# Optimization experiments

Hardware: AMD Instinct MI355X
Metric: run time of the kernel (lower is better)

The kernel has to match this reference:

```python
import jax, jax.numpy as jnp
import numpy as np

V = 32000      # vocab_size
CTX = 1024     # context_length
D = 768        # n_embd
H = 12         # n_heads
HD = D // H    # head_dim
L = 6          # n_layers
DFF = 4 * D
B, S = 2, 1024
EPS = 1e-5


def _layernorm(x, w, b):
    mu = jnp.mean(x, axis=-1, keepdims=True)
    var = jnp.mean(jnp.square(x - mu), axis=-1, keepdims=True)
    return (x - mu) * jax.lax.rsqrt(var + EPS) * w + b


def setup_inputs() -> dict:
    key = jax.random.key(0)
    ks = iter(jax.random.split(key, 32))
    s = 0.02
    idx = jax.random.randint(next(ks), (B, S), 0, V)
    p = {
        "idx": idx,
        "tok_emb": jax.random.normal(next(ks), (V, D), jnp.float32) * s,
        "pos_emb": jax.random.normal(next(ks), (CTX, D), jnp.float32) * s,
        "ln1_w": jnp.ones((L, D)), "ln1_b": jnp.zeros((L, D)),
        "Wq": jax.random.normal(next(ks), (L, D, D), jnp.float32) * s,
        "bq": jnp.zeros((L, D)),
        "Wk": jax.random.normal(next(ks), (L, D, D), jnp.float32) * s,
        "bk": jnp.zeros((L, D)),
        "Wv": jax.random.normal(next(ks), (L, D, D), jnp.float32) * s,
        "bv": jnp.zeros((L, D)),
        "Wo": jax.random.normal(next(ks), (L, D, D), jnp.float32) * s,
        "bo": jnp.zeros((L, D)),
        "ln2_w": jnp.ones((L, D)), "ln2_b": jnp.zeros((L, D)),
        "W1": jax.random.normal(next(ks), (L, D, DFF), jnp.float32) * s,
        "b1": jnp.zeros((L, DFF)),
        "W2": jax.random.normal(next(ks), (L, DFF, D), jnp.float32) * s,
        "b2": jnp.zeros((L, D)),
        "lnf_w": jnp.ones((D,)), "lnf_b": jnp.zeros((D,)),
        "lm_head_w": jax.random.normal(next(ks), (D, V), jnp.float32) * s,
    }
    return p


def _forward(idx, tok_emb, pos_emb, ln1_w, ln1_b, Wq, bq, Wk, bk, Wv, bv,
             Wo, bo, ln2_w, ln2_b, W1, b1, W2, b2, lnf_w, lnf_b, lm_head_w):
    b, s = idx.shape
    x = tok_emb[idx] + pos_emb[:s]  # [B,S,D]
    mask = jnp.tril(jnp.ones((s, s), dtype=bool))  # causal
    scale = 1.0 / np.sqrt(HD)
    for l in range(L):
        # --- attention ---
        h = _layernorm(x, ln1_w[l], ln1_b[l])
        q = (h @ Wq[l] + bq[l]).reshape(b, s, H, HD).transpose(0, 2, 1, 3)
        k = (h @ Wk[l] + bk[l]).reshape(b, s, H, HD).transpose(0, 2, 1, 3)
        v = (h @ Wv[l] + bv[l]).reshape(b, s, H, HD).transpose(0, 2, 1, 3)
        att = jnp.einsum('bhqd,bhkd->bhqk', q, k) * scale
        att = jnp.where(mask, att, -jnp.inf)
        att = jax.nn.softmax(att, axis=-1)
        y = jnp.einsum('bhqk,bhkd->bhqd', att, v)
        y = y.transpose(0, 2, 1, 3).reshape(b, s, D)
        x = x + y @ Wo[l] + bo[l]
        # --- MLP ---
        h2 = _layernorm(x, ln2_w[l], ln2_b[l])
        x = x + jax.nn.relu(h2 @ W1[l] + b1[l]) @ W2[l] + b2[l]
    logits = _layernorm(x, lnf_w, lnf_b) @ lm_head_w  # [B,S,V]
    return logits


def reference(idx, tok_emb, pos_emb, ln1_w, ln1_b, Wq, bq, Wk, bk, Wv, bv,
              Wo, bo, ln2_w, ln2_b, W1, b1, W2, b2, lnf_w, lnf_b, lm_head_w):
    return _forward(idx, tok_emb, pos_emb, ln1_w, ln1_b, Wq, bq, Wk, bk, Wv,
                    bv, Wo, bo, ln2_w, ln2_b, W1, b1, W2, b2, lnf_w, lnf_b,
                    lm_head_w)
```

## Files before the change

### kernel.cpp

```cpp
#include <hip/hip_runtime.h>
#include <hip/hip_bf16.h>
#include <math.h>

#define D 768
#define NH 12
#define HD 64
#define NL 6
#define DFF 3072
#define BB 2
#define SS 1024
#define NROWS (BB*SS)
#define VOCAB 32000
#define QKVN (3*D)
#define LN_EPS 1e-5f

typedef __attribute__((ext_vector_type(8))) short bf16x8;
typedef __attribute__((ext_vector_type(4))) float f32x4;

typedef __attribute__((address_space(1))) const unsigned char* gas_ptr;
typedef __attribute__((address_space(3))) unsigned char* las_ptr;

__device__ __forceinline__ void load_lds16(const void* g, void* l) {
    __builtin_amdgcn_global_load_lds((gas_ptr)g, (las_ptr)l, 16, 0, 0);
}

__device__ __forceinline__ void storeOut(float* p, float v) { *p = v; }
__device__ __forceinline__ void storeOut(__hip_bfloat16* p, float v) { *p = __float2bfloat16(v); }
__device__ __forceinline__ ushort f2bs(float f) {
    __hip_bfloat16 h = __float2bfloat16(f);
    return *(ushort*)&h;
}

#define WAIT_VMCNT(n) asm volatile("s_waitcnt vmcnt(" #n ")" ::: "memory")

__global__ void embed_kernel(const int* __restrict__ idx, const float* __restrict__ tok,
                             const float* __restrict__ pos, float* __restrict__ x) {
    int row = blockIdx.x;
    int s = row % SS;
    int t = idx[row];
    for (int c = threadIdx.x; c < D; c += blockDim.x)
        x[row*D + c] = tok[(size_t)t*D + c] + pos[s*D + c];
}

template<typename OT>
__global__ __launch_bounds__(256) void layernorm_kernel(const float* __restrict__ x,
                                                        const float* __restrict__ w,
                                                        const float* __restrict__ b,
                                                        OT* __restrict__ out) {
    int row = blockIdx.x;
    __shared__ float l1[4], l2[4];
    int base = row * D;
    float vals[3];
    float s1 = 0.f, s2 = 0.f;
#pragma unroll
    for (int i = 0; i < 3; i++) {
        float v = x[base + threadIdx.x + i*256];
        vals[i] = v; s1 += v; s2 += v*v;
    }
#pragma unroll
    for (int o = 32; o > 0; o >>= 1) {
        s1 += __shfl_down(s1, o, 64);
        s2 += __shfl_down(s2, o, 64);
    }
    if ((threadIdx.x & 63) == 0) { l1[threadIdx.x >> 6] = s1; l2[threadIdx.x >> 6] = s2; }
    __syncthreads();
    float sum   = l1[0] + l1[1] + l1[2] + l1[3];
    float sumsq = l2[0] + l2[1] + l2[2] + l2[3];
    float mu  = sum * (1.f / D);
    float var = sumsq * (1.f / D) - mu * mu;
    float inv = rsqrtf(var + LN_EPS);
#pragma unroll
    for (int i = 0; i < 3; i++) {
        int c = threadIdx.x + i*256;
        storeOut(&out[base + c], (vals[i] - mu) * inv * w[c] + b[c]);
    }
}

__global__ __launch_bounds__(256) void transpose_cvt(const float* __restrict__ src,
                                                     __hip_bfloat16* __restrict__ dst,
                                                     int K, int N,
                                                     size_t srcLayerStride, size_t dstLayerStride,
                                                     int dstRowOff) {
    int l = blockIdx.z;
    src += (size_t)l * srcLayerStride;
    dst += (size_t)l * dstLayerStride + (size_t)dstRowOff * K;
    __shared__ float t[32][33];
    int k0 = blockIdx.x*32, n0 = blockIdx.y*32;
    int tx = threadIdx.x & 31, ty = threadIdx.x >> 5;
    for (int i = ty; i < 32; i += 8) t[i][tx] = src[(size_t)(k0+i)*N + n0+tx];
    __syncthreads();
    for (int i = ty; i < 32; i += 8) dst[(size_t)(n0+i)*K + k0+tx] = __float2bfloat16(t[tx][i]);
}

__global__ __launch_bounds__(256) void qkvo_trans(const float* __restrict__ Wq,
                                                  const float* __restrict__ Wk,
                                                  const float* __restrict__ Wv,
                                                  const float* __restrict__ Wo,
                                                  __hip_bfloat16* __restrict__ qkvT,
                                                  __hip_bfloat16* __restrict__ WoT) {
    int z = blockIdx.z, l = z >> 2, m = z & 3;
    const float* src = (m==0 ? Wq : m==1 ? Wk : m==2 ? Wv : Wo) + (size_t)l*D*D;
    __hip_bfloat16* dst = (m < 3) ? qkvT + (size_t)l*QKVN*D + (size_t)m*D*D
                                  : WoT  + (size_t)l*D*D;
    __shared__ float t[32][33];
    int k0 = blockIdx.x*32, n0 = blockIdx.y*32;
    int tx = threadIdx.x & 31, ty = threadIdx.x >> 5;
    for (int i = ty; i < 32; i += 8) t[i][tx] = src[(size_t)(k0+i)*D + n0+tx];
    __syncthreads();
    for (int i = ty; i < 32; i += 8) dst[(size_t)(n0+i)*D + k0+tx] = __float2bfloat16(t[tx][i]);
}

__global__ void pack_qkv_bias(const float* __restrict__ bq, const float* __restrict__ bk,
                              const float* __restrict__ bv, float* __restrict__ dst) {
    int l = blockIdx.y;
    int i = blockIdx.x*256 + threadIdx.x;
    dst[l*QKVN + i]         = bq[l*D + i];
    dst[l*QKVN + D + i]     = bk[l*D + i];
    dst[l*QKVN + 2*D + i]   = bv[l*D + i];
}

#define GSTAGE(buf, k0) do {                                                     \
    _Pragma("unroll")                                                            \
    for (int i_ = 0; i_ < BM/64; i_++) {                                         \
        int rt_ = wid*(BM/4) + i_*16;                                            \
        load_lds16(A + (size_t)(bm + rt_ + lrow)*K + (k0) + lcol,                \
                   &As[buf][rt_][0]);                                            \
    }                                                                            \
    _Pragma("unroll")                                                            \
    for (int i_ = 0; i_ < BN/64; i_++) {                                         \
        int rt_ = wid*(BN/4) + i_*16;                                            \
        load_lds16(BT + (size_t)(bn + rt_ + lrow)*K + (k0) + lcol,               \
                   &Bs[buf][rt_][0]);                                            \
    } } while (0)

template<int BM, int BN, int CMAJ, typename OT, int RELU, int RESID, int HASB, int VSTORE>
__global__ __launch_bounds__(256) void gemm_mfma(const ushort* __restrict__ A,
                                                 const ushort* __restrict__ BT,
                                                 const float* __restrict__ bias,
                                                 const float* __restrict__ X,
                                                 OT* __restrict__ C,
                                                 ushort* __restrict__ vt,
                                                 int N, int K, int gx, int gy) {
    constexpr int WTM = BM/2, WTN = BN/2;
    constexpr int FRM = BM/32, FRN = BN/32;
    __shared__ ushort As[2][BM][32];
    __shared__ ushort Bs[2][BN][32];

    int id = blockIdx.x;
    int swz = (id & 7) * (gridDim.x >> 3) + (id >> 3);
    int bx, by;
    if (CMAJ) { bx = swz / gy; by = swz - bx * gy; }
    else      { by = swz / gx; bx = swz - by * gx; }
    int bm = by * BM, bn = bx * BN;

    int tid = threadIdx.x;
    int lane = tid & 63, wid = tid >> 6;
    int wr = wid >> 1, wc = wid & 1;
    int lrow = lane >> 2;
    int lcol = (((lane & 3) ^ (lrow & 3)) * 8);
    int fr = lane & 15, fc = lane >> 4;

    f32x4 acc[FRM][FRN];
#pragma unroll
    for (int i = 0; i < FRM; i++)
#pragma unroll
        for (int j = 0; j < FRN; j++)
#pragma unroll
            for (int r = 0; r < 4; r++) acc[i][j][r] = 0.f;

    GSTAGE(0, 0);
    asm volatile("s_waitcnt vmcnt(0)" ::: "memory");
    __syncthreads();

    int cur = 0;
    for (int t = 0; t < K/32; t++) {
        if (t*32 + 32 < K) GSTAGE(cur^1, t*32 + 32);
        bf16x8 af[FRM], bf[FRN];
#pragma unroll
        for (int mi = 0; mi < FRM; mi++)
            af[mi] = *(const bf16x8*)&As[cur][wr*WTM + mi*16 + fr][(fc ^ (fr & 3))*8];
#pragma unroll
        for (int ni = 0; ni < FRN; ni++)
            bf[ni] = *(const bf16x8*)&Bs[cur][wc*WTN + ni*16 + fr][(fc ^ (fr & 3))*8];
        __builtin_amdgcn_s_setprio(1);
#pragma unroll
        for (int mi = 0; mi < FRM; mi++)
#pragma unroll
            for (int ni = 0; ni < FRN; ni++)
                acc[mi][ni] = __builtin_amdgcn_mfma_f32_16x16x32_bf16(af[mi], bf[ni], acc[mi][ni], 0, 0, 0);
        __builtin_amdgcn_s_setprio(0);
        asm volatile("s_waitcnt vmcnt(0)" ::: "memory");
        __syncthreads();
        cur ^= 1;
    }

    if (VSTORE && bn >= 2*D) {
        int hh = (bn - 2*D) / HD;
        int b  = bm >> 10;
        size_t vbase = ((size_t)(b*NH + hh)) * HD;
        int srow0 = (bm & (SS-1)) + wr*WTM + fc*4;
#pragma unroll
        for (int mi = 0; mi < FRM; mi++) {
#pragma unroll
            for (int ni = 0; ni < FRN; ni++) {
                int col = bn + wc*WTN + ni*16 + fr;
                int d   = wc*WTN + ni*16 + fr;
                float bv_ = bias[col];
                ushort4 u;
                u.x = f2bs(acc[mi][ni][0] + bv_);
                u.y = f2bs(acc[mi][ni][1] + bv_);
                u.z = f2bs(acc[mi][ni][2] + bv_);
                u.w = f2bs(acc[mi][ni][3] + bv_);
                *(ushort4*)&vt[(vbase + d)*SS + srow0 + mi*16] = u;
            }
        }
    } else {
#pragma unroll
        for (int mi = 0; mi < FRM; mi++) {
#pragma unroll
            for (int r = 0; r < 4; r++) {
                int row = bm + wr*WTM + mi*16 + fc*4 + r;
#pragma unroll
                for (int ni = 0; ni < FRN; ni++) {
                    int col = bn + wc*WTN + ni*16 + fr;
                    float v = acc[mi][ni][r];
                    if (HASB) v += bias[col];
                    if (RESID) v += X[(size_t)row * N + col];
                    if (RELU) v = fmaxf(v, 0.f);
                    storeOut(&C[(size_t)row * N + col], v);
                }
            }
        }
    }
}

#define LGS(buf, k0) do {                                                         \
    _Pragma("unroll")                                                             \
    for (int i_ = 0; i_ < 4; i_++) {                                              \
        int li_ = i_*512 + tid;                                                   \
        int row_ = li_ >> 3;                                                      \
        int kc_ = ((li_ & 7) ^ (row_ & 7)) * 8;                                   \
        size_t doff_ = (size_t)(i_*512 + wid*64) * 8;                             \
        load_lds16(A  + (size_t)(bm + row_)*D + (k0) + kc_,                       \
                   (ushort*)As + (size_t)(buf)*256*64 + doff_);                   \
        load_lds16(BT + (size_t)(bn + row_)*D + (k0) + kc_,                       \
                   (ushort*)Bs + (size_t)(buf)*256*64 + doff_);                   \
    } } while (0)

__global__ __launch_bounds__(512) void lm256_gemm(const ushort* __restrict__ A,
                                                  const ushort* __restrict__ BT,
                                                  float* __restrict__ C) {
    constexpr int NT = D / 64;
    __shared__ ushort As[2][256][64];
    __shared__ ushort Bs[2][256][64];

    int id = blockIdx.x;
    int swz = (id & 7) * 125 + (id >> 3);
    int by = swz & 7;
    int bx = swz >> 3;
    int bm = by * 256, bn = bx * 256;

    int tid = threadIdx.x;
    int lane = tid & 63, wid = tid >> 6;
    int wr = wid >> 2, wc = wid & 3;
    int fr = lane & 15, fc = lane >> 4;

    f32x4 acc[8][4];
#pragma unroll
    for (int i = 0; i < 8; i++)
#pragma unroll
        for (int j = 0; j < 4; j++)
#pragma unroll
            for (int r = 0; r < 4; r++) acc[i][j][r] = 0.f;

    LGS(0, 0);
    LGS(1, 64);
    WAIT_VMCNT(8);
    __builtin_amdgcn_s_barrier();

    for (int t = 0; t < NT; t++) {
        int buf = t & 1;
        bf16x8 bfr[2][4];
#pragma unroll
        for (int kk = 0; kk < 2; kk++)
#pragma unroll
            for (int ni = 0; ni < 4; ni++)
                bfr[kk][ni] = *(const bf16x8*)&Bs[buf][wc*64 + ni*16 + fr][((kk*4 + fc) ^ (fr & 7))*8];
        __builtin_amdgcn_s_setprio(1);
#pragma unroll
        for (int mi = 0; mi < 8; mi++) {
            bf16x8 a0 = *(const bf16x8*)&As[buf][wr*128 + mi*16 + fr][((0 + fc) ^ (fr & 7))*8];
            bf16x8 a1 = *(const bf16x8*)&As[buf][wr*128 + mi*16 + fr][((4 + fc) ^ (fr & 7))*8];
#pragma unroll
            for (int ni = 0; ni < 4; ni++) {
                acc[mi][ni] = __builtin_amdgcn_mfma_f32_16x16x32_bf16(a0, bfr[0][ni], acc[mi][ni], 0, 0, 0);
                acc[mi][ni] = __builtin_amdgcn_mfma_f32_16x16x32_bf16(a1, bfr[1][ni], acc[mi][ni], 0, 0, 0);
            }
        }
        __builtin_amdgcn_s_setprio(0);
        __builtin_amdgcn_s_barrier();
        asm volatile("" ::: "memory");
        if (t + 2 < NT) LGS(buf, (t+2)*64);
        if (t + 1 < NT) {
            if (t + 2 < NT) WAIT_VMCNT(8);
            else            WAIT_VMCNT(0);
            __builtin_amdgcn_s_barrier();
        }
    }

#pragma unroll
    for (int mi = 0; mi < 8; mi++)
#pragma unroll
        for (int r = 0; r < 4; r++) {
            int row = bm + wr*128 + mi*16 + fc*4 + r;
            float* cp = C + (size_t)row * VOCAB + bn + wc*64 + fr;
#pragma unroll
            for (int ni = 0; ni < 4; ni++)
                cp[ni*16] = acc[mi][ni][r];
        }
}

#define KVSTAGE(buf, kv0) do {                                                   \
    _Pragma("unroll")                                                            \
    for (int j_ = 0; j_ < 2; j_++) {                                             \
        int r_ = w*16 + j_*8 + srow8;                                            \
        load_lds16(qkv + (size_t)(b*SS + (kv0) + r_)*QKVN + D + h*HD + schunk*8, \
                   &Ks[buf][w*16 + j_*8][0]);                                    \
        load_lds16(vt + ((size_t)(b*NH + h)*HD + r_)*SS + (kv0) + schunk*8,      \
                   &Vs[buf][w*16 + j_*8][0]);                                    \
    } } while (0)

__global__ __launch_bounds__(256) void attn_mfma(const ushort* __restrict__ qkv,
                                                 const ushort* __restrict__ vt,
                                                 __hip_bfloat16* __restrict__ y) {
    const int bx = blockIdx.x;
    const int qt = 15 - (bx & 15);
    const int h  = (bx >> 4) % NH;
    const int b  = bx / (16*NH);
    const int tid  = threadIdx.x;
    const int lane = tid & 63, w = tid >> 6;
    const int fr = lane & 15, fc = lane >> 4;

    __shared__ ushort Qs[64][64];
    __shared__ ushort Ks[2][64][64];
    __shared__ ushort Vs[2][64][64];
    __shared__ ushort Ps[4][16][72];

    const int q0 = qt * 64;
    const int srow8  = lane >> 3;
    const int schunk = (lane & 7) ^ srow8;

#pragma unroll
    for (int j = 0; j < 2; j++) {
        int r = w*16 + j*8 + srow8;
        load_lds16(qkv + (size_t)(b*SS + q0 + r)*QKVN + h*HD + schunk*8, &Qs[w*16 + j*8][0]);
    }
    KVSTAGE(0, 0);
    asm volatile("s_waitcnt vmcnt(0)" ::: "memory");
    __syncthreads();
    bf16x8 qf[2];
#pragma unroll
    for (int s = 0; s < 2; s++)
        qf[s] = *(const bf16x8*)&Qs[w*16 + fr][((s*4 + fc) ^ (fr & 7))*8];

    f32x4 oacc[4];
#pragma unroll
    for (int ni = 0; ni < 4; ni++)
#pragma unroll
        for (int r = 0; r < 4; r++) oacc[ni][r] = 0.f;
    float m[4] = {-INFINITY, -INFINITY, -INFINITY, -INFINITY};
    float l[4] = {0.f, 0.f, 0.f, 0.f};

    int cur = 0;
    for (int kt = 0; kt <= qt; kt++) {
        if (kt < qt) KVSTAGE(cur^1, (kt+1)*64);
        f32x4 sacc[4];
#pragma unroll
        for (int ni = 0; ni < 4; ni++)
#pragma unroll
            for (int r = 0; r < 4; r++) sacc[ni][r] = 0.f;
#pragma unroll
        for (int ni = 0; ni < 4; ni++)
#pragma unroll
            for (int s = 0; s < 2; s++) {
                bf16x8 kf = *(const bf16x8*)&Ks[cur][ni*16 + fr][((s*4 + fc) ^ (fr & 7))*8];
                sacc[ni] = __builtin_amdgcn_mfma_f32_16x16x32_bf16(qf[s], kf, sacc[ni], 0, 0, 0);
            }
        if (kt == qt) {
#pragma unroll
            for (int ni = 0; ni < 4; ni++)
#pragma unroll
                for (int r = 0; r < 4; r++) {
                    float v = sacc[ni][r] * 0.125f;
                    sacc[ni][r] = (ni*16 + fr > w*16 + fc*4 + r) ? -INFINITY : v;
                }
        } else {
#pragma unroll
            for (int ni = 0; ni < 4; ni++)
#pragma unroll
                for (int r = 0; r < 4; r++) sacc[ni][r] *= 0.125f;
        }
        float p[4][4];
#pragma unroll
        for (int r = 0; r < 4; r++) {
            float mx = fmaxf(fmaxf(sacc[0][r], sacc[1][r]), fmaxf(sacc[2][r], sacc[3][r]));
#pragma unroll
            for (int o = 1; o < 16; o <<= 1) mx = fmaxf(mx, __shfl_xor(mx, o, 64));
            float mn = fmaxf(m[r], mx);
            float fac = __expf(m[r] - mn);
            float rs = 0.f;
#pragma unroll
            for (int ni = 0; ni < 4; ni++) {
                float pv = __expf(sacc[ni][r] - mn);
                p[ni][r] = pv;
                rs += pv;
            }
#pragma unroll
            for (int o = 1; o < 16; o <<= 1) rs += __shfl_xor(rs, o, 64);
            l[r] = l[r] * fac + rs;
            m[r] = mn;
#pragma unroll
            for (int ni = 0; ni < 4; ni++) oacc[ni][r] *= fac;
        }
#pragma unroll
        for (int ni = 0; ni < 4; ni++)
#pragma unroll
            for (int r = 0; r < 4; r++)
                Ps[w][fc*4 + r][ni*16 + fr] = f2bs(p[ni][r]);
        bf16x8 pa[2];
#pragma unroll
        for (int s = 0; s < 2; s++) pa[s] = *(const bf16x8*)&Ps[w][fr][s*32 + fc*8];
#pragma unroll
        for (int ni = 0; ni < 4; ni++)
#pragma unroll
            for (int s = 0; s < 2; s++) {
                bf16x8 vf = *(const bf16x8*)&Vs[cur][ni*16 + fr][((s*4 + fc) ^ (fr & 7))*8];
                oacc[ni] = __builtin_amdgcn_mfma_f32_16x16x32_bf16(pa[s], vf, oacc[ni], 0, 0, 0);
            }
        asm volatile("s_waitcnt vmcnt(0)" ::: "memory");
        __syncthreads();
        cur ^= 1;
    }
#pragma unroll
    for (int r = 0; r < 4; r++) {
        float rinv = 1.f / l[r];
        int row = b*SS + q0 + w*16 + fc*4 + r;
#pragma unroll
        for (int ni = 0; ni < 4; ni++)
            y[(size_t)row*D + h*HD + ni*16 + fr] = __float2bfloat16(oacc[ni][r] * rinv);
    }
}

extern "C" void kernel_launch(void* const* d_in, const int* in_sizes, int n_in,
                              void* d_out, int out_size, void* d_ws, size_t ws_size,
                              hipStream_t stream) {
    const int*   idx  = (const int*)d_in[0];
    const float* tok  = (const float*)d_in[1];
    const float* pos  = (const float*)d_in[2];
    const float* ln1w = (const float*)d_in[3];
    const float* ln1b = (const float*)d_in[4];
    const float* Wq   = (const float*)d_in[5];
    const float* bq   = (const float*)d_in[6];
    const float* Wk   = (const float*)d_in[7];
    const float* bk   = (const float*)d_in[8];
    const float* Wv   = (const float*)d_in[9];
    const float* bv   = (const float*)d_in[10];
    const float* Wo   = (const float*)d_in[11];
    const float* bo   = (const float*)d_in[12];
    const float* ln2w = (const float*)d_in[13];
    const float* ln2b = (const float*)d_in[14];
    const float* W1   = (const float*)d_in[15];
    const float* b1   = (const float*)d_in[16];
    const float* W2   = (const float*)d_in[17];
    const float* b2   = (const float*)d_in[18];
    const float* lnfw = (const float*)d_in[19];
    const float* lnfb = (const float*)d_in[20];
    const float* lmw  = (const float*)d_in[21];
    float* out = (float*)d_out;

    char* p = (char*)d_ws;
    __hip_bfloat16* qkvT = (__hip_bfloat16*)p; p += (size_t)NL*QKVN*D*2;
    __hip_bfloat16* WoT  = (__hip_bfloat16*)p; p += (size_t)NL*D*D*2;
    __hip_bfloat16* W1T  = (__hip_bfloat16*)p; p += (size_t)NL*DFF*D*2;
    __hip_bfloat16* W2T  = (__hip_bfloat16*)p; p += (size_t)NL*D*DFF*2;
    __hip_bfloat16* lmT  = (__hip_bfloat16*)p; p += (size_t)VOCAB*D*2;
    float*          bqkv = (float*)p;          p += (size_t)NL*QKVN*4;
    float*          x    = (float*)p;          p += (size_t)NROWS*D*4;
    __hip_bfloat16* h    = (__hip_bfloat16*)p; p += (size_t)NROWS*D*2;
    __hip_bfloat16* qkv  = (__hip_bfloat16*)p; p += (size_t)NROWS*QKVN*2;
    __hip_bfloat16* vt   = (__hip_bfloat16*)p; p += (size_t)BB*NH*HD*SS*2;
    __hip_bfloat16* yb   = (__hip_bfloat16*)p; p += (size_t)NROWS*D*2;
    __hip_bfloat16* a1   = (__hip_bfloat16*)p; p += (size_t)NROWS*DFF*2;

    qkvo_trans<<<dim3(D/32, D/32, NL*4), 256, 0, stream>>>(Wq, Wk, Wv, Wo, qkvT, WoT);
    transpose_cvt<<<dim3(D/32, DFF/32, NL), 256, 0, stream>>>(W1, W1T, D, DFF, (size_t)D*DFF, (size_t)DFF*D, 0);
    transpose_cvt<<<dim3(DFF/32, D/32, NL), 256, 0, stream>>>(W2, W2T, DFF, D, (size_t)DFF*D, (size_t)D*DFF, 0);
    transpose_cvt<<<dim3(D/32, VOCAB/32, 1), 256, 0, stream>>>(lmw, lmT, D, VOCAB, 0, 0, 0);
    pack_qkv_bias<<<dim3(3, NL), 256, 0, stream>>>(bq, bk, bv, bqkv);

    embed_kernel<<<NROWS, 256, 0, stream>>>(idx, tok, pos, x);

    for (int l = 0; l < NL; l++) {
        layernorm_kernel<<<NROWS, 256, 0, stream>>>(x, ln1w + l*D, ln1b + l*D, h);
        gemm_mfma<128,64,0,__hip_bfloat16,0,0,1,1><<<576, 256, 0, stream>>>(
            (const ushort*)h, (const ushort*)(qkvT + (size_t)l*QKVN*D),
            bqkv + (size_t)l*QKVN, nullptr, qkv, (ushort*)vt, QKVN, D, QKVN/64, NROWS/128);
        attn_mfma<<<BB*NH*(SS/64), 256, 0, stream>>>((const ushort*)qkv, (const ushort*)vt, yb);
        gemm_mfma<64,64,0,float,0,1,1,0><<<384, 256, 0, stream>>>(
            (const ushort*)yb, (const ushort*)(WoT + (size_t)l*D*D),
            bo + (size_t)l*D, x, x, nullptr, D, D, D/64, NROWS/64);
        layernorm_kernel<<<NROWS, 256, 0, stream>>>(x, ln2w + l*D, ln2b + l*D, h);
        gemm_mfma<128,128,0,__hip_bfloat16,1,0,1,0><<<384, 256, 0, stream>>>(
            (const ushort*)h, (const ushort*)(W1T + (size_t)l*DFF*D),
            b1 + (size_t)l*DFF, nullptr, a1, nullptr, DFF, D, DFF/128, NROWS/128);
        gemm_mfma<64,64,0,float,0,1,1,0><<<384, 256, 0, stream>>>(
            (const ushort*)a1, (const ushort*)(W2T + (size_t)l*D*DFF),
            b2 + (size_t)l*D, x, x, nullptr, D, DFF, D/64, NROWS/64);
    }
    layernorm_kernel<<<NROWS, 256, 0, stream>>>(x, lnfw, lnfb, h);
    lm256_gemm<<<1000, 512, 0, stream>>>((const ushort*)h, (const ushort*)lmT, out);
}
```

Measured before the change: 1.243 ms.

## Use 4-slot LDS ring pipelines for residual and LM-head GEMMs with new swizzle

```diff
diff --git a/kernel.cpp b/kernel.cpp
--- a/kernel.cpp
+++ b/kernel.cpp
@@ -119,6 +119,7 @@
     dst[l*QKVN + 2*D + i]   = bv[l*D + i];
 }
 
+
 #define GSTAGE(buf, k0) do {                                                     \
     _Pragma("unroll")                                                            \
     for (int i_ = 0; i_ < BM/64; i_++) {                                         \
@@ -157,8 +158,9 @@
     int lane = tid & 63, wid = tid >> 6;
     int wr = wid >> 1, wc = wid & 1;
     int lrow = lane >> 2;
-    int lcol = (((lane & 3) ^ (lrow & 3)) * 8);
+    int lcol = (((lane & 3) ^ ((lane >> 3) & 3)) * 8);
     int fr = lane & 15, fc = lane >> 4;
+    int rchunk = (fc ^ ((fr >> 1) & 3)) * 8;
 
     f32x4 acc[FRM][FRN];
 #pragma unroll
@@ -178,10 +180,10 @@
         bf16x8 af[FRM], bf[FRN];
 #pragma unroll
         for (int mi = 0; mi < FRM; mi++)
-            af[mi] = *(const bf16x8*)&As[cur][wr*WTM + mi*16 + fr][(fc ^ (fr & 3))*8];
+            af[mi] = *(const bf16x8*)&As[cur][wr*WTM + mi*16 + fr][rchunk];
 #pragma unroll
         for (int ni = 0; ni < FRN; ni++)
-            bf[ni] = *(const bf16x8*)&Bs[cur][wc*WTN + ni*16 + fr][(fc ^ (fr & 3))*8];
+            bf[ni] = *(const bf16x8*)&Bs[cur][wc*WTN + ni*16 + fr][rchunk];
         __builtin_amdgcn_s_setprio(1);
 #pragma unroll
         for (int mi = 0; mi < FRM; mi++)
@@ -234,25 +236,106 @@
     }
 }
 
-#define LGS(buf, k0) do {                                                         \
+#define RSTAGE(slot, k0) do {                                                    \
+    int row_ = tid >> 2;                                                         \
+    load_lds16(A  + (size_t)(bm + row_)*K + (k0) + sc_,                          \
+               (char*)As + (size_t)(slot)*4096 + (size_t)wid*1024);              \
+    load_lds16(BT + (size_t)(bn + row_)*K + (k0) + sc_,                          \
+               (char*)Bs + (size_t)(slot)*4096 + (size_t)wid*1024);              \
+    } while (0)
+
+template<int RELU>
+__global__ __launch_bounds__(256) void gemm_ring64(const ushort* __restrict__ A,
+                                                   const ushort* __restrict__ BT,
+                                                   const float* __restrict__ bias,
+                                                   const float* __restrict__ X,
+                                                   float* __restrict__ C,
+                                                   int N, int K, int gx) {
+    __shared__ ushort As[4][64][32];
+    __shared__ ushort Bs[4][64][32];
+
+    int id = blockIdx.x;
+    int swz = (id & 7) * (gridDim.x >> 3) + (id >> 3);
+    int by = swz / gx, bx = swz - by * gx;
+    int bm = by * 64, bn = bx * 64;
+
+    int tid = threadIdx.x;
+    int lane = tid & 63, wid = tid >> 6;
+    int wr = wid >> 1, wc = wid & 1;
+    int sc_ = ((lane & 3) ^ ((lane >> 3) & 3)) * 8;
+    int fr = lane & 15, fc = lane >> 4;
+    int rchunk = (fc ^ ((fr >> 1) & 3)) * 8;
+
+    f32x4 acc[2][2];
+#pragma unroll
+    for (int i = 0; i < 2; i++)
+#pragma unroll
+        for (int j = 0; j < 2; j++)
+#pragma unroll
+            for (int r = 0; r < 4; r++) acc[i][j][r] = 0.f;
+
+    const int NT = K / 32;
+    RSTAGE(0, 0);
+    RSTAGE(1, 32);
+    RSTAGE(2, 64);
+
+    for (int t = 0; t < NT; t++) {
+        if (t < NT-2)      WAIT_VMCNT(4);
+        else if (t == NT-2) WAIT_VMCNT(2);
+        else               WAIT_VMCNT(0);
+        __builtin_amdgcn_s_barrier();
+        asm volatile("" ::: "memory");
+        if (t + 3 < NT) RSTAGE((t+3) & 3, (t+3)*32);
+        int s = t & 3;
+        bf16x8 af[2], bf[2];
+#pragma unroll
+        for (int mi = 0; mi < 2; mi++)
+            af[mi] = *(const bf16x8*)&As[s][wr*32 + mi*16 + fr][rchunk];
+#pragma unroll
+        for (int ni = 0; ni < 2; ni++)
+            bf[ni] = *(const bf16x8*)&Bs[s][wc*32 + ni*16 + fr][rchunk];
+        __builtin_amdgcn_s_setprio(1);
+#pragma unroll
+        for (int mi = 0; mi < 2; mi++)
+#pragma unroll
+            for (int ni = 0; ni < 2; ni++)
+                acc[mi][ni] = __builtin_amdgcn_mfma_f32_16x16x32_bf16(af[mi], bf[ni], acc[mi][ni], 0, 0, 0);
+        __builtin_amdgcn_s_setprio(0);
+    }
+
+#pragma unroll
+    for (int mi = 0; mi < 2; mi++) {
+#pragma unroll
+        for (int r = 0; r < 4; r++) {
+            int row = bm + wr*32 + mi*16 + fc*4 + r;
+#pragma unroll
+            for (int ni = 0; ni < 2; ni++) {
+                int col = bn + wc*32 + ni*16 + fr;
+                float v = acc[mi][ni][r] + bias[col] + X[(size_t)row * N + col];
+                if (RELU) v = fmaxf(v, 0.f);
+                C[(size_t)row * N + col] = v;
+            }
+        }
+    }
+}
+
+#define LMS(slot, k0) do {                                                        \
     _Pragma("unroll")                                                             \
-    for (int i_ = 0; i_ < 4; i_++) {                                              \
-        int li_ = i_*512 + tid;                                                   \
-        int row_ = li_ >> 3;                                                      \
-        int kc_ = ((li_ & 7) ^ (row_ & 7)) * 8;                                   \
-        size_t doff_ = (size_t)(i_*512 + wid*64) * 8;                             \
-        load_lds16(A  + (size_t)(bm + row_)*D + (k0) + kc_,                       \
-                   (ushort*)As + (size_t)(buf)*256*64 + doff_);                   \
-        load_lds16(BT + (size_t)(bn + row_)*D + (k0) + kc_,                       \
-                   (ushort*)Bs + (size_t)(buf)*256*64 + doff_);                   \
+    for (int i_ = 0; i_ < 2; i_++) {                                              \
+        int row_ = i_*128 + (tid >> 2);                                           \
+        size_t db_ = (size_t)(i_*512 + wid*64) * 16;                              \
+        load_lds16(A  + (size_t)(bm + row_)*D + (k0) + sc_,                       \
+                   (char*)As + (size_t)(slot)*16384 + db_);                       \
+        load_lds16(BT + (size_t)(bn + row_)*D + (k0) + sc_,                       \
+                   (char*)Bs + (size_t)(slot)*16384 + db_);                       \
     } } while (0)
 
 __global__ __launch_bounds__(512) void lm256_gemm(const ushort* __restrict__ A,
                                                   const ushort* __restrict__ BT,
                                                   float* __restrict__ C) {
-    constexpr int NT = D / 64;
-    __shared__ ushort As[2][256][64];
-    __shared__ ushort Bs[2][256][64];
+    constexpr int NT = D / 32;
+    __shared__ ushort As[4][256][32];
+    __shared__ ushort Bs[4][256][32];
 
     int id = blockIdx.x;
     int swz = (id & 7) * 125 + (id >> 3);
@@ -263,7 +346,9 @@
     int tid = threadIdx.x;
     int lane = tid & 63, wid = tid >> 6;
     int wr = wid >> 2, wc = wid & 3;
+    int sc_ = ((tid & 3) ^ ((tid >> 3) & 3)) * 8;
     int fr = lane & 15, fc = lane >> 4;
+    int rchunk = (fc ^ ((fr >> 1) & 3)) * 8;
 
     f32x4 acc[8][4];
 #pragma unroll
@@ -273,39 +358,31 @@
 #pragma unroll
             for (int r = 0; r < 4; r++) acc[i][j][r] = 0.f;
 
-    LGS(0, 0);
-    LGS(1, 64);
-    WAIT_VMCNT(8);
-    __builtin_amdgcn_s_barrier();
+    LMS(0, 0);
+    LMS(1, 32);
+    LMS(2, 64);
 
     for (int t = 0; t < NT; t++) {
-        int buf = t & 1;
-        bf16x8 bfr[2][4];
-#pragma unroll
-        for (int kk = 0; kk < 2; kk++)
-#pragma unroll
-            for (int ni = 0; ni < 4; ni++)
-                bfr[kk][ni] = *(const bf16x8*)&Bs[buf][wc*64 + ni*16 + fr][((kk*4 + fc) ^ (fr & 7))*8];
-        __builtin_amdgcn_s_setprio(1);
-#pragma unroll
-        for (int mi = 0; mi < 8; mi++) {
-            bf16x8 a0 = *(const bf16x8*)&As[buf][wr*128 + mi*16 + fr][((0 + fc) ^ (fr & 7))*8];
-            bf16x8 a1 = *(const bf16x8*)&As[buf][wr*128 + mi*16 + fr][((4 + fc) ^ (fr & 7))*8];
-#pragma unroll
-            for (int ni = 0; ni < 4; ni++) {
-                acc[mi][ni] = __builtin_amdgcn_mfma_f32_16x16x32_bf16(a0, bfr[0][ni], acc[mi][ni], 0, 0, 0);
-                acc[mi][ni] = __builtin_amdgcn_mfma_f32_16x16x32_bf16(a1, bfr[1][ni], acc[mi][ni], 0, 0, 0);
-            }
-        }
-        __builtin_amdgcn_s_setprio(0);
+        if (t < NT-2)      WAIT_VMCNT(8);
+        else if (t == NT-2) WAIT_VMCNT(4);
+        else               WAIT_VMCNT(0);
         __builtin_amdgcn_s_barrier();
         asm volatile("" ::: "memory");
-        if (t + 2 < NT) LGS(buf, (t+2)*64);
-        if (t + 1 < NT) {
-            if (t + 2 < NT) WAIT_VMCNT(8);
-            else            WAIT_VMCNT(0);
-            __builtin_amdgcn_s_barrier();
-        }
+        if (t + 3 < NT) LMS((t+3) & 3, (t+3)*32);
+        int s = t & 3;
+        bf16x8 bfr[4];
+#pragma unroll
+        for (int ni = 0; ni < 4; ni++)
+            bfr[ni] = *(const bf16x8*)&Bs[s][wc*64 + ni*16 + fr][rchunk];
+        __builtin_amdgcn_s_setprio(1);
+#pragma unroll
+        for (int mi = 0; mi < 8; mi++) {
+            bf16x8 a0 = *(const bf16x8*)&As[s][wr*128 + mi*16 + fr][rchunk];
+#pragma unroll
+            for (int ni = 0; ni < 4; ni++)
+                acc[mi][ni] = __builtin_amdgcn_mfma_f32_16x16x32_bf16(a0, bfr[ni], acc[mi][ni], 0, 0, 0);
+        }
+        __builtin_amdgcn_s_setprio(0);
     }
 
 #pragma unroll
@@ -506,16 +583,16 @@
             (const ushort*)h, (const ushort*)(qkvT + (size_t)l*QKVN*D),
             bqkv + (size_t)l*QKVN, nullptr, qkv, (ushort*)vt, QKVN, D, QKVN/64, NROWS/128);
         attn_mfma<<<BB*NH*(SS/64), 256, 0, stream>>>((const ushort*)qkv, (const ushort*)vt, yb);
-        gemm_mfma<64,64,0,float,0,1,1,0><<<384, 256, 0, stream>>>(
+        gemm_ring64<0><<<384, 256, 0, stream>>>(
             (const ushort*)yb, (const ushort*)(WoT + (size_t)l*D*D),
-            bo + (size_t)l*D, x, x, nullptr, D, D, D/64, NROWS/64);
+            bo + (size_t)l*D, x, x, D, D, D/64);
         layernorm_kernel<<<NROWS, 256, 0, stream>>>(x, ln2w + l*D, ln2b + l*D, h);
         gemm_mfma<128,128,0,__hip_bfloat16,1,0,1,0><<<384, 256, 0, stream>>>(
             (const ushort*)h, (const ushort*)(W1T + (size_t)l*DFF*D),
             b1 + (size_t)l*DFF, nullptr, a1, nullptr, DFF, D, DFF/128, NROWS/128);
-        gemm_mfma<64,64,0,float,0,1,1,0><<<384, 256, 0, stream>>>(
+        gemm_ring64<0><<<384, 256, 0, stream>>>(
             (const ushort*)a1, (const ushort*)(W2T + (size_t)l*D*DFF),
-            b2 + (size_t)l*D, x, x, nullptr, D, DFF, D/64, NROWS/64);
+            b2 + (size_t)l*D, x, x, D, DFF, D/64);
     }
     layernorm_kernel<<<NROWS, 256, 0, stream>>>(x, lnfw, lnfb, h);
     lm256_gemm<<<1000, 512, 0, stream>>>((const ushort*)h, (const ushort*)lmT, out);
```

New measurement: 1.232 ms. Within noise of the previous version (-0.9%).
